# Kernel tuning notes

Hardware: AMD Instinct MI355X
Metric: run time of the kernel (lower is better)

## Reference

```python
import jax, jax.numpy as jnp
import numpy as np

ALPHA = 0.2        # LeakyReLU negative slope
OUT_FEATURE = 256
NEG_INF = -1e9


def setup_inputs() -> dict:
    key = jax.random.key(0)
    k1, k2, k3, k4 = jax.random.split(key, 4)
    N, F_IN, F_OUT = 8192, 512, OUT_FEATURE
    x = jax.random.normal(k1, (N, F_IN), dtype=jnp.float32)
    adj = jax.random.randint(k2, (N, N), 0, 2, dtype=jnp.int32)
    # Xavier-uniform-ish params
    W = jax.random.normal(k3, (F_IN, F_OUT), dtype=jnp.float32) * (1.414 / np.sqrt(F_IN))
    a = jax.random.normal(k4, (2 * F_OUT, 1), dtype=jnp.float32) * (1.414 / np.sqrt(2 * F_OUT))
    return {"x": x, "adj": adj, "W": W, "a": a}


def reference(x, adj, W, a):
    # x: [N, F_in], adj: [N, N] int, W: [F_in, F_out], a: [2*F_out, 1]
    h = x @ W                                   # [N, F_out]
    a_src = a[:OUT_FEATURE, 0]                  # [F_out]
    a_dst = a[OUT_FEATURE:, 0]                  # [F_out]
    e_i = h @ a_src                             # [N]
    e_j = h @ a_dst                             # [N]
    e = e_i[:, None] + e_j[None, :]             # [N, N] additive scores
    e = jnp.where(e > 0, e, ALPHA * e)          # LeakyReLU
    e = jnp.where(adj <= 0, NEG_INF, e)         # mask non-edges
    attn = jax.nn.softmax(e, axis=-1)           # row-wise softmax
    out = attn @ h                              # [N, F_out] aggregate
    return jax.nn.elu(out)                      # dropout is identity in eval
```

## Files before the change

### kernel.cpp

```cpp
#include <hip/hip_runtime.h>
#include <hip/hip_fp16.h>

#define N_NODES 8192
#define F_IN    512
#define F_OUT   256
#define LOG2E   1.4426950408889634f

typedef __attribute__((ext_vector_type(8))) _Float16 half8;
typedef __attribute__((ext_vector_type(2))) __fp16   fp16x2;
typedef __attribute__((ext_vector_type(4))) float    f32x4;

union H8U4 { half8 h; uint4 u; };
union H2U  { fp16x2 h; unsigned u; };

__global__ __launch_bounds__(256) void k_badj(const int* __restrict__ adj,
                                              unsigned long long* __restrict__ bm) {
  const int nw   = (gridDim.x * 256) >> 6;
  const int gw   = (blockIdx.x * 256 + threadIdx.x) >> 6;
  const int lane = threadIdx.x & 63;
  const int nchunk = N_NODES * (N_NODES / 64);
  for (int c0 = gw * 4; c0 < nchunk; c0 += nw * 4) {
    const size_t base = (size_t)c0 * 64 + lane;
    const int v0 = __builtin_nontemporal_load(adj + base);
    const int v1 = __builtin_nontemporal_load(adj + base + 64);
    const int v2 = __builtin_nontemporal_load(adj + base + 128);
    const int v3 = __builtin_nontemporal_load(adj + base + 192);
    const unsigned long long m0 = __ballot(v0 > 0);
    const unsigned long long m1 = __ballot(v1 > 0);
    const unsigned long long m2 = __ballot(v2 > 0);
    const unsigned long long m3 = __ballot(v3 > 0);
    if (lane == 0) {
      uint4 s0, s1;
      s0.x = (unsigned)m0; s0.y = (unsigned)(m0 >> 32);
      s0.z = (unsigned)m1; s0.w = (unsigned)(m1 >> 32);
      s1.x = (unsigned)m2; s1.y = (unsigned)(m2 >> 32);
      s1.z = (unsigned)m3; s1.w = (unsigned)(m3 >> 32);
      *(uint4*)(bm + c0)     = s0;
      *(uint4*)(bm + c0 + 2) = s1;
    }
  }
}

__global__ __launch_bounds__(256) void k_prep(const float* __restrict__ W,
                                              unsigned short* __restrict__ wph,
                                              unsigned short* __restrict__ wpl,
                                              unsigned* __restrict__ emax_u) {
  const int gid = blockIdx.x * 256 + threadIdx.x;
  if (gid == 0) *emax_u = 0u;
  const int k = gid >> 8;
  const int c = gid & 255;
  const float w = W[(size_t)k * F_OUT + c];
  const _Float16 hi = (_Float16)w;
  const _Float16 lo = (_Float16)(w - (float)hi);
  const size_t idx =
      (((size_t)(k >> 5) * 16 + (c >> 4)) * 64 + (c & 15) + 16 * ((k >> 3) & 3)) * 8 +
      (k & 7);
  wph[idx] = *(const unsigned short*)&hi;
  wpl[idx] = *(const unsigned short*)&lo;
}

__global__ __launch_bounds__(512) void k_hgemm(const float* __restrict__ x,
                                               const uint4* __restrict__ wph4,
                                               const uint4* __restrict__ wpl4,
                                               const float* __restrict__ a,
                                               unsigned short* __restrict__ hpack,
                                               float* __restrict__ EI,
                                               float* __restrict__ EJ,
                                               unsigned* __restrict__ emax_u) {
  __shared__ float eip[4][32], ejp[4][32], emx[32];
  const int r0   = blockIdx.x * 32;
  const int tid  = threadIdx.x;
  const int wid  = tid >> 6, lane = tid & 63;
  const int mg   = wid >> 2, ng = wid & 3;
  const int lo16 = lane & 15, hi4 = lane >> 4;

  const float* xrow = x + (size_t)(r0 + mg * 16 + lo16) * F_IN + hi4 * 8;
  const uint4* whb = wph4 + (size_t)(ng * 4) * 64 + lane;
  const uint4* wlb = wpl4 + (size_t)(ng * 4) * 64 + lane;

  f32x4 acc[4] = {};

  float4 xa = *(const float4*)(xrow);
  float4 xb = *(const float4*)(xrow + 4);
  uint4 wh[4], wl[4];
#pragma unroll
  for (int nf = 0; nf < 4; ++nf) {
    wh[nf] = whb[(size_t)nf * 64];
    wl[nf] = wlb[(size_t)nf * 64];
  }

#pragma unroll
  for (int ks = 0; ks < 16; ++ks) {
    H8U4 ah, al;
    const float v[8] = {xa.x, xa.y, xa.z, xa.w, xb.x, xb.y, xb.z, xb.w};
#pragma unroll
    for (int j = 0; j < 8; ++j) {
      const _Float16 h = (_Float16)v[j];
      ah.h[j] = h;
      al.h[j] = (_Float16)(v[j] - (float)h);
    }
    if (ks + 1 < 16) {
      xa = *(const float4*)(xrow + (ks + 1) * 32);
      xb = *(const float4*)(xrow + (ks + 1) * 32 + 4);
    }
#pragma unroll
    for (int nf = 0; nf < 4; ++nf) {
      H8U4 bh, bl;
      bh.u = wh[nf];
      bl.u = wl[nf];
      acc[nf] = __builtin_amdgcn_mfma_f32_16x16x32_f16(ah.h, bh.h, acc[nf], 0, 0, 0);
      acc[nf] = __builtin_amdgcn_mfma_f32_16x16x32_f16(al.h, bh.h, acc[nf], 0, 0, 0);
      acc[nf] = __builtin_amdgcn_mfma_f32_16x16x32_f16(ah.h, bl.h, acc[nf], 0, 0, 0);
    }
    if (ks + 1 < 16) {
#pragma unroll
      for (int nf = 0; nf < 4; ++nf) {
        wh[nf] = whb[(size_t)((ks + 1) * 16 + nf) * 64];
        wl[nf] = wlb[(size_t)((ks + 1) * 16 + nf) * 64];
      }
    }
  }

  float asv[4], adv[4];
#pragma unroll
  for (int nf = 0; nf < 4; ++nf) {
    const int c = ng * 64 + nf * 16 + lo16;
    asv[nf] = a[c];
    adv[nf] = a[F_OUT + c];
  }
#pragma unroll
  for (int q = 0; q < 4; ++q) {
    float s1 = acc[0][q] * asv[0] + acc[1][q] * asv[1] + acc[2][q] * asv[2] +
               acc[3][q] * asv[3];
    float s2 = acc[0][q] * adv[0] + acc[1][q] * adv[1] + acc[2][q] * adv[2] +
               acc[3][q] * adv[3];
#pragma unroll
    for (int o = 1; o < 16; o <<= 1) {
      s1 += __shfl_xor(s1, o);
      s2 += __shfl_xor(s2, o);
    }
    if (lo16 == 0) {
      const int rl = mg * 16 + hi4 * 4 + q;
      eip[ng][rl] = s1;
      ejp[ng][rl] = s2;
    }
  }

#pragma unroll
  for (int nf = 0; nf < 4; ++nf) {
#pragma unroll
    for (int q = 0; q < 4; ++q) {
      const int row = r0 + mg * 16 + hi4 * 4 + q;
      const int col = ng * 64 + nf * 16 + lo16;
      const size_t idx =
          (((size_t)(row >> 5) * 16 + (col >> 4)) * 64 + (col & 15) +
           16 * ((row >> 3) & 3)) * 8 + (row & 7);
      const _Float16 hv = (_Float16)acc[nf][q];
      hpack[idx] = *(const unsigned short*)&hv;
    }
  }

  __syncthreads();
  if (tid < 32) {
    const float s1 = eip[0][tid] + eip[1][tid] + eip[2][tid] + eip[3][tid];
    const float s2 = ejp[0][tid] + ejp[1][tid] + ejp[2][tid] + ejp[3][tid];
    const int row = r0 + tid;
    EI[row] = s1 * LOG2E;
    const float e2 = s2 * LOG2E;
    EJ[row] = e2;
    emx[tid] = e2;
  }
  __syncthreads();
  if (tid == 0) {
    float m = emx[0];
#pragma unroll
    for (int i = 1; i < 32; ++i) m = fmaxf(m, emx[i]);
    unsigned b = __float_as_uint(m);
    unsigned u = (b & 0x80000000u) ? ~b : (b | 0x80000000u);
    atomicMax(emax_u, u);
  }
}

__global__ __launch_bounds__(512, 4) void k_pv(const unsigned char* __restrict__ bmask,
                                               const uint4* __restrict__ hp4,
                                               const float* __restrict__ EI,
                                               const float* __restrict__ EJ,
                                               const unsigned* __restrict__ emax_u,
                                               float* __restrict__ npart,
                                               float* __restrict__ dpart,
                                               int ntiles) {
  __shared__ __align__(16) uint4 ps4[8 * 64];
  __shared__ float ejhi[2048], ejlo[2048];
  __shared__ float A1[64], A2[64], den[64];
  const int rowbase = blockIdx.x * 64;
  const int split   = blockIdx.y;
  const int jt0     = split * ntiles;
  const int tid     = threadIdx.x;
  const int wid  = tid >> 6, lane = tid & 63;
  const int lo   = lane & 15, hi = lane >> 4;

  float EMAX;
  {
    const unsigned u = *emax_u;
    EMAX = (u & 0x80000000u) ? __uint_as_float(u & 0x7fffffffu) : __uint_as_float(~u);
  }
  if (tid < 64) {
    const float e  = EI[rowbase + tid];
    const float s  = e + EMAX;
    const float mi = fmaxf(s, 0.2f * s);
    A1[tid] = e - mi;
    A2[tid] = 0.2f * e - mi;
    den[tid] = 0.f;
  }
  const bool uselds = (ntiles <= 32);
  if (uselds) {
    int eidx = jt0 * 64 + tid * 4;
    if (eidx > N_NODES - 4) eidx = N_NODES - 4;
    const float4 ev = *(const float4*)&EJ[eidx];
    *(float4*)&ejhi[tid * 4] = ev;
    float4 el = {0.2f * ev.x, 0.2f * ev.y, 0.2f * ev.z, 0.2f * ev.w};
    *(float4*)&ejlo[tid * 4] = el;
  }
  __syncthreads();

  const int msub = wid & 3, ksw = wid >> 2;
  const int row_p = msub * 16 + lo;
  const int jloc  = ksw * 32 + hi * 8;
  const float a1r = A1[row_p], a2r = A2[row_p];
  const unsigned char* mbp =
      bmask + (size_t)(rowbase + row_p) * (N_NODES / 8) + (size_t)jt0 * 8 + ksw * 4 + hi;
  const float* ejg  = EJ + jt0 * 64 + jloc;
  const int mg = wid >> 2, ng = wid & 3;
  const uint4* hb = hp4 + (ng * 4) * 64 + lane;

  f32x4 acc[2][4] = {};
  float dacc = 0.f;

  unsigned mcur = mbp[0];
  unsigned mnxt = (ntiles > 1) ? (unsigned)mbp[8] : 0u;

  for (int jt = 0; jt < ntiles; ++jt) {
    const int tb = (jt0 + jt) * 2048;
    const uint4 b00 = hb[tb + 0 * 1024 + 0 * 64];
    const uint4 b01 = hb[tb + 0 * 1024 + 1 * 64];
    const uint4 b02 = hb[tb + 0 * 1024 + 2 * 64];
    const uint4 b03 = hb[tb + 0 * 1024 + 3 * 64];
    const uint4 b10 = hb[tb + 1 * 1024 + 0 * 64];
    const uint4 b11 = hb[tb + 1 * 1024 + 1 * 64];
    const uint4 b12 = hb[tb + 1 * 1024 + 2 * 64];
    const uint4 b13 = hb[tb + 1 * 1024 + 3 * 64];

    float eh[8], el[8];
    if (uselds) {
      const float4 h0 = *(const float4*)&ejhi[jt * 64 + jloc];
      const float4 h1 = *(const float4*)&ejhi[jt * 64 + jloc + 4];
      const float4 l0 = *(const float4*)&ejlo[jt * 64 + jloc];
      const float4 l1 = *(const float4*)&ejlo[jt * 64 + jloc + 4];
      eh[0]=h0.x; eh[1]=h0.y; eh[2]=h0.z; eh[3]=h0.w;
      eh[4]=h1.x; eh[5]=h1.y; eh[6]=h1.z; eh[7]=h1.w;
      el[0]=l0.x; el[1]=l0.y; el[2]=l0.z; el[3]=l0.w;
      el[4]=l1.x; el[5]=l1.y; el[6]=l1.z; el[7]=l1.w;
    } else {
      const float4 e0 = *(const float4*)(ejg + jt * 64);
      const float4 e1 = *(const float4*)(ejg + jt * 64 + 4);
      eh[0]=e0.x; eh[1]=e0.y; eh[2]=e0.z; eh[3]=e0.w;
      eh[4]=e1.x; eh[5]=e1.y; eh[6]=e1.z; eh[7]=e1.w;
#pragma unroll
      for (int j = 0; j < 8; ++j) el[j] = 0.2f * eh[j];
    }
    float ph[8];
#pragma unroll
    for (int j = 0; j < 8; ++j) {
      const float s = fmaxf(eh[j] + a1r, el[j] + a2r);
      const float p = __builtin_amdgcn_exp2f(s);
      ph[j] = (mcur & (1u << j)) ? p : 0.f;
    }
    dacc += ((ph[0] + ph[1]) + (ph[2] + ph[3])) + ((ph[4] + ph[5]) + (ph[6] + ph[7]));
    H2U q0, q1, q2, q3;
    q0.h = __builtin_amdgcn_cvt_pkrtz(ph[0], ph[1]);
    q1.h = __builtin_amdgcn_cvt_pkrtz(ph[2], ph[3]);
    q2.h = __builtin_amdgcn_cvt_pkrtz(ph[4], ph[5]);
    q3.h = __builtin_amdgcn_cvt_pkrtz(ph[6], ph[7]);
    uint4 pk = {q0.u, q1.u, q2.u, q3.u};

    asm volatile("" ::: "memory");
    __builtin_amdgcn_s_barrier();
    asm volatile("" ::: "memory");
    ps4[wid * 64 + lane] = pk;
    mcur = mnxt;
    if (jt + 2 < ntiles) mnxt = (unsigned)mbp[(jt + 2) * 8];
    asm volatile("s_waitcnt lgkmcnt(0)" ::: "memory");
    __builtin_amdgcn_s_barrier();
    asm volatile("" ::: "memory");

    H8U4 a00, a01, a10, a11;
    a00.u = ps4[(0 * 4 + mg * 2 + 0) * 64 + lane];
    a10.u = ps4[(0 * 4 + mg * 2 + 1) * 64 + lane];
    a01.u = ps4[(1 * 4 + mg * 2 + 0) * 64 + lane];
    a11.u = ps4[(1 * 4 + mg * 2 + 1) * 64 + lane];
    H8U4 b;
    __builtin_amdgcn_s_setprio(1);
    b.u = b00;
    acc[0][0] = __builtin_amdgcn_mfma_f32_16x16x32_f16(a00.h, b.h, acc[0][0], 0, 0, 0);
    acc[1][0] = __builtin_amdgcn_mfma_f32_16x16x32_f16(a10.h, b.h, acc[1][0], 0, 0, 0);
    b.u = b01;
    acc[0][1] = __builtin_amdgcn_mfma_f32_16x16x32_f16(a00.h, b.h, acc[0][1], 0, 0, 0);
    acc[1][1] = __builtin_amdgcn_mfma_f32_16x16x32_f16(a10.h, b.h, acc[1][1], 0, 0, 0);
    b.u = b02;
    acc[0][2] = __builtin_amdgcn_mfma_f32_16x16x32_f16(a00.h, b.h, acc[0][2], 0, 0, 0);
    acc[1][2] = __builtin_amdgcn_mfma_f32_16x16x32_f16(a10.h, b.h, acc[1][2], 0, 0, 0);
    b.u = b03;
    acc[0][3] = __builtin_amdgcn_mfma_f32_16x16x32_f16(a00.h, b.h, acc[0][3], 0, 0, 0);
    acc[1][3] = __builtin_amdgcn_mfma_f32_16x16x32_f16(a10.h, b.h, acc[1][3], 0, 0, 0);
    b.u = b10;
    acc[0][0] = __builtin_amdgcn_mfma_f32_16x16x32_f16(a01.h, b.h, acc[0][0], 0, 0, 0);
    acc[1][0] = __builtin_amdgcn_mfma_f32_16x16x32_f16(a11.h, b.h, acc[1][0], 0, 0, 0);
    b.u = b11;
    acc[0][1] = __builtin_amdgcn_mfma_f32_16x16x32_f16(a01.h, b.h, acc[0][1], 0, 0, 0);
    acc[1][1] = __builtin_amdgcn_mfma_f32_16x16x32_f16(a11.h, b.h, acc[1][1], 0, 0, 0);
    b.u = b12;
    acc[0][2] = __builtin_amdgcn_mfma_f32_16x16x32_f16(a01.h, b.h, acc[0][2], 0, 0, 0);
    acc[1][2] = __builtin_amdgcn_mfma_f32_16x16x32_f16(a11.h, b.h, acc[1][2], 0, 0, 0);
    b.u = b13;
    acc[0][3] = __builtin_amdgcn_mfma_f32_16x16x32_f16(a01.h, b.h, acc[0][3], 0, 0, 0);
    acc[1][3] = __builtin_amdgcn_mfma_f32_16x16x32_f16(a11.h, b.h, acc[1][3], 0, 0, 0);
    __builtin_amdgcn_s_setprio(0);
  }

  atomicAdd(&den[row_p], dacc);
  __syncthreads();

  float* npb = npart + (size_t)split * N_NODES * F_OUT;
#pragma unroll
  for (int mi_ = 0; mi_ < 2; ++mi_) {
    const int rb = rowbase + (mg * 2 + mi_) * 16 + hi * 4;
#pragma unroll
    for (int nf = 0; nf < 4; ++nf) {
      const int col = ng * 64 + nf * 16 + lo;
#pragma unroll
      for (int r2 = 0; r2 < 4; ++r2)
        __builtin_nontemporal_store(acc[mi_][nf][r2],
                                    &npb[(size_t)(rb + r2) * F_OUT + col]);
    }
  }
  if (tid < 64)
    __builtin_nontemporal_store(den[tid],
                                &dpart[(size_t)split * N_NODES + rowbase + tid]);
}

__global__ __launch_bounds__(256) void k_fin(const float* __restrict__ npart,
                                             const float* __restrict__ dpart,
                                             float* __restrict__ out,
                                             int nsplit) {
  const int gid = blockIdx.x * 256 + threadIdx.x;
  const int row = gid >> 6;
  const int c4  = (gid & 63) << 2;
  f32x4 s = {0.f, 0.f, 0.f, 0.f};
  float d = 0.f;
  for (int sp = 0; sp < nsplit; ++sp) {
    const f32x4 v = __builtin_nontemporal_load(
        (const f32x4*)(npart + ((size_t)sp * N_NODES + row) * F_OUT + c4));
    s += v;
    d += dpart[(size_t)sp * N_NODES + row];
  }
  const float inv = 1.f / d;
  float o[4] = {s.x * inv, s.y * inv, s.z * inv, s.w * inv};
#pragma unroll
  for (int i = 0; i < 4; ++i) o[i] = (o[i] > 0.f) ? o[i] : expm1f(o[i]);
  float4 ov = {o[0], o[1], o[2], o[3]};
  *(float4*)(out + (size_t)row * F_OUT + c4) = ov;
}

extern "C" void kernel_launch(void* const* d_in, const int* in_sizes, int n_in,
                              void* d_out, int out_size, void* d_ws, size_t ws_size,
                              hipStream_t stream) {
  const float* x   = (const float*)d_in[0];
  const int*   adj = (const int*)d_in[1];
  const float* W   = (const float*)d_in[2];
  const float* a   = (const float*)d_in[3];
  float* out = (float*)d_out;
  char*  ws  = (char*)d_ws;

  unsigned short* hpack = (unsigned short*)ws;
  size_t off = (size_t)4 * 1024 * 1024;
  float* EI = (float*)(ws + off); off += (size_t)N_NODES * 4;
  float* EJ = (float*)(ws + off); off += (size_t)N_NODES * 4;
  unsigned* emax_u = (unsigned*)(ws + off); off += 256;
  float* dpart = (float*)(ws + off); off += (size_t)8 * N_NODES * 4;
  unsigned short* wph = (unsigned short*)(ws + off); off += (size_t)F_IN * F_OUT * 2;
  unsigned short* wpl = (unsigned short*)(ws + off); off += (size_t)F_IN * F_OUT * 2;
  unsigned long long* bmask = (unsigned long long*)(ws + off);
  off += (size_t)N_NODES * (N_NODES / 8);
  float* npart = (float*)(ws + off);

  int nsplit = 4;
  while (nsplit > 1 && off + (size_t)nsplit * N_NODES * F_OUT * 4 > ws_size) nsplit >>= 1;

  k_badj<<<dim3(2048), dim3(256), 0, stream>>>(adj, bmask);
  k_prep<<<dim3((F_IN * F_OUT) / 256), dim3(256), 0, stream>>>(W, wph, wpl, emax_u);
  k_hgemm<<<dim3(N_NODES / 32), dim3(512), 0, stream>>>(
      x, (const uint4*)wph, (const uint4*)wpl, a, hpack, EI, EJ, emax_u);
  k_pv<<<dim3(128, nsplit), dim3(512), 0, stream>>>(
      (const unsigned char*)bmask, (const uint4*)hpack, EI, EJ, emax_u, npart, dpart,
      128 / nsplit);
  k_fin<<<dim3(N_NODES * 64 / 256), dim3(256), 0, stream>>>(npart, dpart, out, nsplit);
}
```

Measured before the change: 144.5 us.

## Fuse adjacency bitmask into h GEMM and factor softmax exp into per-node terms

```diff
diff --git a/kernel.cpp b/kernel.cpp
--- a/kernel.cpp
+++ b/kernel.cpp
@@ -9,37 +9,10 @@
 typedef __attribute__((ext_vector_type(8))) _Float16 half8;
 typedef __attribute__((ext_vector_type(2))) __fp16   fp16x2;
 typedef __attribute__((ext_vector_type(4))) float    f32x4;
+typedef __attribute__((ext_vector_type(4))) int      i32x4;
 
 union H8U4 { half8 h; uint4 u; };
 union H2U  { fp16x2 h; unsigned u; };
-
-__global__ __launch_bounds__(256) void k_badj(const int* __restrict__ adj,
-                                              unsigned long long* __restrict__ bm) {
-  const int nw   = (gridDim.x * 256) >> 6;
-  const int gw   = (blockIdx.x * 256 + threadIdx.x) >> 6;
-  const int lane = threadIdx.x & 63;
-  const int nchunk = N_NODES * (N_NODES / 64);
-  for (int c0 = gw * 4; c0 < nchunk; c0 += nw * 4) {
-    const size_t base = (size_t)c0 * 64 + lane;
-    const int v0 = __builtin_nontemporal_load(adj + base);
-    const int v1 = __builtin_nontemporal_load(adj + base + 64);
-    const int v2 = __builtin_nontemporal_load(adj + base + 128);
-    const int v3 = __builtin_nontemporal_load(adj + base + 192);
-    const unsigned long long m0 = __ballot(v0 > 0);
-    const unsigned long long m1 = __ballot(v1 > 0);
-    const unsigned long long m2 = __ballot(v2 > 0);
-    const unsigned long long m3 = __ballot(v3 > 0);
-    if (lane == 0) {
-      uint4 s0, s1;
-      s0.x = (unsigned)m0; s0.y = (unsigned)(m0 >> 32);
-      s0.z = (unsigned)m1; s0.w = (unsigned)(m1 >> 32);
-      s1.x = (unsigned)m2; s1.y = (unsigned)(m2 >> 32);
-      s1.z = (unsigned)m3; s1.w = (unsigned)(m3 >> 32);
-      *(uint4*)(bm + c0)     = s0;
-      *(uint4*)(bm + c0 + 2) = s1;
-    }
-  }
-}
 
 __global__ __launch_bounds__(256) void k_prep(const float* __restrict__ W,
                                               unsigned short* __restrict__ wph,
@@ -59,18 +32,51 @@
   wpl[idx] = *(const unsigned short*)&lo;
 }
 
-__global__ __launch_bounds__(512) void k_hgemm(const float* __restrict__ x,
-                                               const uint4* __restrict__ wph4,
-                                               const uint4* __restrict__ wpl4,
-                                               const float* __restrict__ a,
-                                               unsigned short* __restrict__ hpack,
-                                               float* __restrict__ EI,
-                                               float* __restrict__ EJ,
-                                               unsigned* __restrict__ emax_u) {
+__global__ __launch_bounds__(512) void k_hb(const float* __restrict__ x,
+                                            const uint4* __restrict__ wph4,
+                                            const uint4* __restrict__ wpl4,
+                                            const float* __restrict__ a,
+                                            const int* __restrict__ adj,
+                                            unsigned short* __restrict__ hpack,
+                                            float* __restrict__ EI,
+                                            float* __restrict__ EJ,
+                                            float* __restrict__ U,
+                                            float* __restrict__ V,
+                                            unsigned* __restrict__ emax_u,
+                                            unsigned long long* __restrict__ bm) {
   __shared__ float eip[4][32], ejp[4][32], emx[32];
-  const int r0   = blockIdx.x * 32;
   const int tid  = threadIdx.x;
   const int wid  = tid >> 6, lane = tid & 63;
+
+  if (blockIdx.x >= N_NODES / 32) {
+    const int bb = blockIdx.x - N_NODES / 32;
+    const int nw = 512 * 8;
+    const int gw = bb * 8 + wid;
+    const int nchunk = N_NODES * (N_NODES / 64);
+    for (int c0 = gw * 4; c0 < nchunk; c0 += nw * 4) {
+      const size_t base = (size_t)c0 * 64 + lane;
+      const int v0 = __builtin_nontemporal_load(adj + base);
+      const int v1 = __builtin_nontemporal_load(adj + base + 64);
+      const int v2 = __builtin_nontemporal_load(adj + base + 128);
+      const int v3 = __builtin_nontemporal_load(adj + base + 192);
+      const unsigned long long m0 = __ballot(v0 > 0);
+      const unsigned long long m1 = __ballot(v1 > 0);
+      const unsigned long long m2 = __ballot(v2 > 0);
+      const unsigned long long m3 = __ballot(v3 > 0);
+      if (lane == 0) {
+        uint4 s0, s1;
+        s0.x = (unsigned)m0; s0.y = (unsigned)(m0 >> 32);
+        s0.z = (unsigned)m1; s0.w = (unsigned)(m1 >> 32);
+        s1.x = (unsigned)m2; s1.y = (unsigned)(m2 >> 32);
+        s1.z = (unsigned)m3; s1.w = (unsigned)(m3 >> 32);
+        *(uint4*)(bm + c0)     = s0;
+        *(uint4*)(bm + c0 + 2) = s1;
+      }
+    }
+    return;
+  }
+
+  const int r0   = blockIdx.x * 32;
   const int mg   = wid >> 2, ng = wid & 3;
   const int lo16 = lane & 15, hi4 = lane >> 4;
 
@@ -168,6 +174,8 @@
     EI[row] = s1 * LOG2E;
     const float e2 = s2 * LOG2E;
     EJ[row] = e2;
+    U[row] = __builtin_amdgcn_exp2f(e2);
+    V[row] = __builtin_amdgcn_exp2f(0.2f * e2);
     emx[tid] = e2;
   }
   __syncthreads();
@@ -181,17 +189,17 @@
   }
 }
 
-__global__ __launch_bounds__(512, 4) void k_pv(const unsigned char* __restrict__ bmask,
+__global__ __launch_bounds__(512, 4) void k_pv(const unsigned long long* __restrict__ bm,
                                                const uint4* __restrict__ hp4,
                                                const float* __restrict__ EI,
-                                               const float* __restrict__ EJ,
+                                               const float* __restrict__ U,
+                                               const float* __restrict__ V,
                                                const unsigned* __restrict__ emax_u,
                                                float* __restrict__ npart,
                                                float* __restrict__ dpart,
                                                int ntiles) {
-  __shared__ __align__(16) uint4 ps4[8 * 64];
-  __shared__ float ejhi[2048], ejlo[2048];
-  __shared__ float A1[64], A2[64], den[64];
+  __shared__ float ul[2048], vl[2048];
+  __shared__ float c1s[64], c2s[64], den[64];
   const int rowbase = blockIdx.x * 64;
   const int split   = blockIdx.y;
   const int jt0     = split * ntiles;
@@ -208,126 +216,133 @@
     const float e  = EI[rowbase + tid];
     const float s  = e + EMAX;
     const float mi = fmaxf(s, 0.2f * s);
-    A1[tid] = e - mi;
-    A2[tid] = 0.2f * e - mi;
+    c1s[tid] = __builtin_amdgcn_exp2f(e - mi);
+    c2s[tid] = __builtin_amdgcn_exp2f(0.2f * e - mi);
     den[tid] = 0.f;
   }
   const bool uselds = (ntiles <= 32);
   if (uselds) {
     int eidx = jt0 * 64 + tid * 4;
     if (eidx > N_NODES - 4) eidx = N_NODES - 4;
-    const float4 ev = *(const float4*)&EJ[eidx];
-    *(float4*)&ejhi[tid * 4] = ev;
-    float4 el = {0.2f * ev.x, 0.2f * ev.y, 0.2f * ev.z, 0.2f * ev.w};
-    *(float4*)&ejlo[tid * 4] = el;
+    *(float4*)&ul[tid * 4] = *(const float4*)&U[eidx];
+    *(float4*)&vl[tid * 4] = *(const float4*)&V[eidx];
   }
   __syncthreads();
 
-  const int msub = wid & 3, ksw = wid >> 2;
-  const int row_p = msub * 16 + lo;
-  const int jloc  = ksw * 32 + hi * 8;
-  const float a1r = A1[row_p], a2r = A2[row_p];
-  const unsigned char* mbp =
-      bmask + (size_t)(rowbase + row_p) * (N_NODES / 8) + (size_t)jt0 * 8 + ksw * 4 + hi;
-  const float* ejg  = EJ + jt0 * 64 + jloc;
   const int mg = wid >> 2, ng = wid & 3;
+  const int r0l = mg * 32 + lo, r1l = r0l + 16;
+  const float c1r0 = c1s[r0l], c2r0 = c2s[r0l];
+  const float c1r1 = c1s[r1l], c2r1 = c2s[r1l];
+  const unsigned long long* bm0 =
+      bm + (size_t)(rowbase + r0l) * (N_NODES / 64) + jt0;
+  const unsigned long long* bm1 =
+      bm + (size_t)(rowbase + r1l) * (N_NODES / 64) + jt0;
   const uint4* hb = hp4 + (ng * 4) * 64 + lane;
+  const float* ug = U + jt0 * 64;
+  const float* vg = V + jt0 * 64;
 
   f32x4 acc[2][4] = {};
-  float dacc = 0.f;
-
-  unsigned mcur = mbp[0];
-  unsigned mnxt = (ntiles > 1) ? (unsigned)mbp[8] : 0u;
+  float dacc0 = 0.f, dacc1 = 0.f;
+
+  unsigned long long m0c = bm0[0], m1c = bm1[0];
+
+  auto mk = [&](const float* uu, const float* vv, unsigned mw, float c1, float c2,
+                float& dac) -> uint4 {
+    float p[8];
+#pragma unroll
+    for (int e = 0; e < 8; ++e) {
+      const float pm = fmaxf(uu[e] * c1, vv[e] * c2);
+      p[e] = ((mw >> e) & 1u) ? pm : 0.f;
+    }
+    dac += ((p[0] + p[1]) + (p[2] + p[3])) + ((p[4] + p[5]) + (p[6] + p[7]));
+    H2U q0, q1, q2, q3;
+    q0.h = __builtin_amdgcn_cvt_pkrtz(p[0], p[1]);
+    q1.h = __builtin_amdgcn_cvt_pkrtz(p[2], p[3]);
+    q2.h = __builtin_amdgcn_cvt_pkrtz(p[4], p[5]);
+    q3.h = __builtin_amdgcn_cvt_pkrtz(p[6], p[7]);
+    uint4 r = {q0.u, q1.u, q2.u, q3.u};
+    return r;
+  };
 
   for (int jt = 0; jt < ntiles; ++jt) {
     const int tb = (jt0 + jt) * 2048;
-    const uint4 b00 = hb[tb + 0 * 1024 + 0 * 64];
-    const uint4 b01 = hb[tb + 0 * 1024 + 1 * 64];
-    const uint4 b02 = hb[tb + 0 * 1024 + 2 * 64];
-    const uint4 b03 = hb[tb + 0 * 1024 + 3 * 64];
-    const uint4 b10 = hb[tb + 1 * 1024 + 0 * 64];
-    const uint4 b11 = hb[tb + 1 * 1024 + 1 * 64];
-    const uint4 b12 = hb[tb + 1 * 1024 + 2 * 64];
-    const uint4 b13 = hb[tb + 1 * 1024 + 3 * 64];
-
-    float eh[8], el[8];
+    uint4 b0[4];
+#pragma unroll
+    for (int f = 0; f < 4; ++f) b0[f] = hb[tb + f * 64];
+
+    unsigned long long m0n = 0, m1n = 0;
+    if (jt + 1 < ntiles) { m0n = bm0[jt + 1]; m1n = bm1[jt + 1]; }
+
+    float u0[8], v0[8], u1[8], v1[8];
     if (uselds) {
-      const float4 h0 = *(const float4*)&ejhi[jt * 64 + jloc];
-      const float4 h1 = *(const float4*)&ejhi[jt * 64 + jloc + 4];
-      const float4 l0 = *(const float4*)&ejlo[jt * 64 + jloc];
-      const float4 l1 = *(const float4*)&ejlo[jt * 64 + jloc + 4];
-      eh[0]=h0.x; eh[1]=h0.y; eh[2]=h0.z; eh[3]=h0.w;
-      eh[4]=h1.x; eh[5]=h1.y; eh[6]=h1.z; eh[7]=h1.w;
-      el[0]=l0.x; el[1]=l0.y; el[2]=l0.z; el[3]=l0.w;
-      el[4]=l1.x; el[5]=l1.y; el[6]=l1.z; el[7]=l1.w;
+      *(float4*)&u0[0] = *(const float4*)&ul[jt * 64 + hi * 8];
+      *(float4*)&u0[4] = *(const float4*)&ul[jt * 64 + hi * 8 + 4];
+      *(float4*)&v0[0] = *(const float4*)&vl[jt * 64 + hi * 8];
+      *(float4*)&v0[4] = *(const float4*)&vl[jt * 64 + hi * 8 + 4];
+      *(float4*)&u1[0] = *(const float4*)&ul[jt * 64 + 32 + hi * 8];
+      *(float4*)&u1[4] = *(const float4*)&ul[jt * 64 + 32 + hi * 8 + 4];
+      *(float4*)&v1[0] = *(const float4*)&vl[jt * 64 + 32 + hi * 8];
+      *(float4*)&v1[4] = *(const float4*)&vl[jt * 64 + 32 + hi * 8 + 4];
     } else {
-      const float4 e0 = *(const float4*)(ejg + jt * 64);
-      const float4 e1 = *(const float4*)(ejg + jt * 64 + 4);
-      eh[0]=e0.x; eh[1]=e0.y; eh[2]=e0.z; eh[3]=e0.w;
-      eh[4]=e1.x; eh[5]=e1.y; eh[6]=e1.z; eh[7]=e1.w;
-#pragma unroll
-      for (int j = 0; j < 8; ++j) el[j] = 0.2f * eh[j];
-    }
-    float ph[8];
-#pragma unroll
-    for (int j = 0; j < 8; ++j) {
-      const float s = fmaxf(eh[j] + a1r, el[j] + a2r);
-      const float p = __builtin_amdgcn_exp2f(s);
-      ph[j] = (mcur & (1u << j)) ? p : 0.f;
-    }
-    dacc += ((ph[0] + ph[1]) + (ph[2] + ph[3])) + ((ph[4] + ph[5]) + (ph[6] + ph[7]));
-    H2U q0, q1, q2, q3;
-    q0.h = __builtin_amdgcn_cvt_pkrtz(ph[0], ph[1]);
-    q1.h = __builtin_amdgcn_cvt_pkrtz(ph[2], ph[3]);
-    q2.h = __builtin_amdgcn_cvt_pkrtz(ph[4], ph[5]);
-    q3.h = __builtin_amdgcn_cvt_pkrtz(ph[6], ph[7]);
-    uint4 pk = {q0.u, q1.u, q2.u, q3.u};
-
-    asm volatile("" ::: "memory");
-    __builtin_amdgcn_s_barrier();
-    asm volatile("" ::: "memory");
-    ps4[wid * 64 + lane] = pk;
-    mcur = mnxt;
-    if (jt + 2 < ntiles) mnxt = (unsigned)mbp[(jt + 2) * 8];
-    asm volatile("s_waitcnt lgkmcnt(0)" ::: "memory");
-    __builtin_amdgcn_s_barrier();
-    asm volatile("" ::: "memory");
-
-    H8U4 a00, a01, a10, a11;
-    a00.u = ps4[(0 * 4 + mg * 2 + 0) * 64 + lane];
-    a10.u = ps4[(0 * 4 + mg * 2 + 1) * 64 + lane];
-    a01.u = ps4[(1 * 4 + mg * 2 + 0) * 64 + lane];
-    a11.u = ps4[(1 * 4 + mg * 2 + 1) * 64 + lane];
+      *(float4*)&u0[0] = *(const float4*)&ug[jt * 64 + hi * 8];
+      *(float4*)&u0[4] = *(const float4*)&ug[jt * 64 + hi * 8 + 4];
+      *(float4*)&v0[0] = *(const float4*)&vg[jt * 64 + hi * 8];
+      *(float4*)&v0[4] = *(const float4*)&vg[jt * 64 + hi * 8 + 4];
+      *(float4*)&u1[0] = *(const float4*)&ug[jt * 64 + 32 + hi * 8];
+      *(float4*)&u1[4] = *(const float4*)&ug[jt * 64 + 32 + hi * 8 + 4];
+      *(float4*)&v1[0] = *(const float4*)&vg[jt * 64 + 32 + hi * 8];
+      *(float4*)&v1[4] = *(const float4*)&vg[jt * 64 + 32 + hi * 8 + 4];
+    }
+
+    const unsigned mw00 = (unsigned)(m0c >> (hi * 8));
+    const unsigned mw01 = (unsigned)(m0c >> (32 + hi * 8));
+    const unsigned mw10 = (unsigned)(m1c >> (hi * 8));
+    const unsigned mw11 = (unsigned)(m1c >> (32 + hi * 8));
+
+    H8U4 a00, a10, a01, a11;
+    a00.u = mk(u0, v0, mw00, c1r0, c2r0, dacc0);
+    a10.u = mk(u0, v0, mw10, c1r1, c2r1, dacc1);
+    uint4 b1[4];
+#pragma unroll
+    for (int f = 0; f < 4; ++f) b1[f] = hb[tb + 1024 + f * 64];
+    a01.u = mk(u1, v1, mw01, c1r0, c2r0, dacc0);
+    a11.u = mk(u1, v1, mw11, c1r1, c2r1, dacc1);
+
     H8U4 b;
     __builtin_amdgcn_s_setprio(1);
-    b.u = b00;
+    b.u = b0[0];
     acc[0][0] = __builtin_amdgcn_mfma_f32_16x16x32_f16(a00.h, b.h, acc[0][0], 0, 0, 0);
     acc[1][0] = __builtin_amdgcn_mfma_f32_16x16x32_f16(a10.h, b.h, acc[1][0], 0, 0, 0);
-    b.u = b01;
+    b.u = b0[1];
     acc[0][1] = __builtin_amdgcn_mfma_f32_16x16x32_f16(a00.h, b.h, acc[0][1], 0, 0, 0);
     acc[1][1] = __builtin_amdgcn_mfma_f32_16x16x32_f16(a10.h, b.h, acc[1][1], 0, 0, 0);
-    b.u = b02;
+    b.u = b0[2];
     acc[0][2] = __builtin_amdgcn_mfma_f32_16x16x32_f16(a00.h, b.h, acc[0][2], 0, 0, 0);
     acc[1][2] = __builtin_amdgcn_mfma_f32_16x16x32_f16(a10.h, b.h, acc[1][2], 0, 0, 0);
-    b.u = b03;
+    b.u = b0[3];
     acc[0][3] = __builtin_amdgcn_mfma_f32_16x16x32_f16(a00.h, b.h, acc[0][3], 0, 0, 0);
     acc[1][3] = __builtin_amdgcn_mfma_f32_16x16x32_f16(a10.h, b.h, acc[1][3], 0, 0, 0);
-    b.u = b10;
+    b.u = b1[0];
     acc[0][0] = __builtin_amdgcn_mfma_f32_16x16x32_f16(a01.h, b.h, acc[0][0], 0, 0, 0);
     acc[1][0] = __builtin_amdgcn_mfma_f32_16x16x32_f16(a11.h, b.h, acc[1][0], 0, 0, 0);
-    b.u = b11;
+    b.u = b1[1];
     acc[0][1] = __builtin_amdgcn_mfma_f32_16x16x32_f16(a01.h, b.h, acc[0][1], 0, 0, 0);
     acc[1][1] = __builtin_amdgcn_mfma_f32_16x16x32_f16(a11.h, b.h, acc[1][1], 0, 0, 0);
-    b.u = b12;
+    b.u = b1[2];
     acc[0][2] = __builtin_amdgcn_mfma_f32_16x16x32_f16(a01.h, b.h, acc[0][2], 0, 0, 0);
     acc[1][2] = __builtin_amdgcn_mfma_f32_16x16x32_f16(a11.h, b.h, acc[1][2], 0, 0, 0);
-    b.u = b13;
+    b.u = b1[3];
     acc[0][3] = __builtin_amdgcn_mfma_f32_16x16x32_f16(a01.h, b.h, acc[0][3], 0, 0, 0);
     acc[1][3] = __builtin_amdgcn_mfma_f32_16x16x32_f16(a11.h, b.h, acc[1][3], 0, 0, 0);
     __builtin_amdgcn_s_setprio(0);
-  }
-
-  atomicAdd(&den[row_p], dacc);
+
+    m0c = m0n; m1c = m1n;
+  }
+
+  if (ng == 0) {
+    atomicAdd(&den[r0l], dacc0);
+    atomicAdd(&den[r1l], dacc1);
+  }
   __syncthreads();
 
   float* npb = npart + (size_t)split * N_NODES * F_OUT;
@@ -385,6 +400,8 @@
   size_t off = (size_t)4 * 1024 * 1024;
   float* EI = (float*)(ws + off); off += (size_t)N_NODES * 4;
   float* EJ = (float*)(ws + off); off += (size_t)N_NODES * 4;
+  float* U  = (float*)(ws + off); off += (size_t)N_NODES * 4;
+  float* V  = (float*)(ws + off); off += (size_t)N_NODES * 4;
   unsigned* emax_u = (unsigned*)(ws + off); off += 256;
   float* dpart = (float*)(ws + off); off += (size_t)8 * N_NODES * 4;
   unsigned short* wph = (unsigned short*)(ws + off); off += (size_t)F_IN * F_OUT * 2;
@@ -396,12 +413,11 @@
   int nsplit = 4;
   while (nsplit > 1 && off + (size_t)nsplit * N_NODES * F_OUT * 4 > ws_size) nsplit >>= 1;
 
-  k_badj<<<dim3(2048), dim3(256), 0, stream>>>(adj, bmask);
   k_prep<<<dim3((F_IN * F_OUT) / 256), dim3(256), 0, stream>>>(W, wph, wpl, emax_u);
-  k_hgemm<<<dim3(N_NODES / 32), dim3(512), 0, stream>>>(
-      x, (const uint4*)wph, (const uint4*)wpl, a, hpack, EI, EJ, emax_u);
+  k_hb<<<dim3(N_NODES / 32 + 512), dim3(512), 0, stream>>>(
+      x, (const uint4*)wph, (const uint4*)wpl, a, adj, hpack, EI, EJ, U, V, emax_u,
+      bmask);
   k_pv<<<dim3(128, nsplit), dim3(512), 0, stream>>>(
-      (const unsigned char*)bmask, (const uint4*)hpack, EI, EJ, emax_u, npart, dpart,
-      128 / nsplit);
+      bmask, (const uint4*)hpack, EI, U, V, emax_u, npart, dpart, 128 / nsplit);
   k_fin<<<dim3(N_NODES * 64 / 256), dim3(256), 0, stream>>>(npart, dpart, out, nsplit);
 }
```

Measured after the change: 270.0 us. 1.87x slower.
